# Kernel tuning notes

Measured on AMD Instinct MI355X. Metric: run time of the kernel, lower is better.

## Reference

```python
import jax, jax.numpy as jnp
import numpy as np

V = 50000      # vocabulary size (len(negative_sampling_table))
E = 256        # embedding_size
R = 180        # time_scope_radius -> 2R+1 = 361 time buckets
B = 2048       # batch
L = 200        # context length
NOPT = 10      # number of candidate targets (mixed_target has NOPT+1 cols)


def setup_inputs() -> dict:
    key = jax.random.key(0)
    k1, k2, k3, k4, k5, k6 = jax.random.split(key, 6)
    context = jax.random.randint(k1, (B, L, 2), 0, V, dtype=jnp.int64)
    mixed_target = jax.random.randint(k2, (B, NOPT + 1), 0, V, dtype=jnp.int64)
    context_emb_table = jax.random.normal(k3, (V, E), dtype=jnp.float32)
    target_emb_table = jax.random.normal(k4, (V, E), dtype=jnp.float32)
    taa_matrix = jax.random.uniform(k5, (V, 2 * R + 1), dtype=jnp.float32)
    taa_bias = jax.random.uniform(k6, (V, 1), dtype=jnp.float32)
    return {
        "context": context,
        "mixed_target": mixed_target,
        "context_emb_table": context_emb_table,
        "target_emb_table": target_emb_table,
        "taa_matrix": taa_matrix,
        "taa_bias": taa_bias,
    }


def reference(context, mixed_target, context_emb_table, target_emb_table, taa_matrix, taa_bias):
    radius = (taa_matrix.shape[1] - 1) // 2
    context_event = context[:, :, 0]          # [B, L]
    context_time = context[:, :, 1]           # [B, L]
    n_options = mixed_target.shape[-1] - 1
    target_event = mixed_target[:, :n_options]   # [B, n_options]
    target_time = mixed_target[:, n_options:]    # [B, 1]

    # mask padded positions (event id == -1)
    context_mask = jnp.where(context_event == -1, 0, 1)
    context_event = context_event * context_mask

    context_embedding = context_emb_table[context_event]          # [B, L, E]

    time_delta = jnp.clip(context_time - target_time + radius, 0, 2 * radius)  # [B, L]

    activated_taa = jax.nn.softmax(taa_matrix + taa_bias, axis=1)  # [V, 2R+1]
    taa_weights = activated_taa[context_event, time_delta]         # [B, L]

    # weighted masked sum over context positions
    w = taa_weights * context_mask.astype(taa_weights.dtype)       # [B, L]
    hidden = jnp.einsum("ble,bl->be", context_embedding, w)       # [B, E]

    target_embedding = target_emb_table[target_event]              # [B, n_options, E]
    scores = jnp.einsum("bne,be->bn", target_embedding, hidden)   # [B, n_options]
    return scores
```

## Files before the change

kernel.cpp:

```cpp
#include <hip/hip_runtime.h>
#include <hip/hip_bf16.h>

#define V 50000
#define E 256
#define RADIUS 180
#define TAA_W (2 * RADIUS + 1)
#define BATCH 2048
#define CTX_L 200
#define NOPT 10

#define ISE_GROUPS (V / 8)
#define VEC4_TOTAL (V * E / 4)
#define PREP_GRID  2048

typedef float vf4 __attribute__((ext_vector_type(4)));

__device__ __forceinline__ unsigned short f2bf_rne(float f) {
    unsigned u = __float_as_uint(f);
    u += 0x7fffu + ((u >> 16) & 1u);
    return (unsigned short)(u >> 16);
}
__device__ __forceinline__ unsigned pack_bf16(float a, float b) {
    return (unsigned)f2bf_rne(a) | ((unsigned)f2bf_rne(b) << 16);
}
__device__ __forceinline__ float bf_lo(unsigned u) {
    return __uint_as_float(u << 16);
}
__device__ __forceinline__ float bf_hi(unsigned u) {
    return __uint_as_float(u & 0xffff0000u);
}

__global__ __launch_bounds__(256) void prep_persist_kernel(
    const float* __restrict__ taa, const float* __restrict__ ctx_tab,
    float* __restrict__ inv, uint2* __restrict__ btab, int do_conv)
{
    __shared__ float s_e[8 * TAA_W];
    const int tid = threadIdx.x;

    for (int g = blockIdx.x; g < ISE_GROUPS; g += PREP_GRID) {
        const float4* p = (const float4*)taa + (size_t)g * 722;
#pragma unroll
        for (int k = 0; k < 3; ++k) {
            int j = tid + 256 * k;
            if (j < 722) {
                float4 v = p[j];
                float* d = &s_e[4 * j];
                d[0] = __expf(v.x);
                d[1] = __expf(v.y);
                d[2] = __expf(v.z);
                d[3] = __expf(v.w);
            }
        }
        __syncthreads();
        const int r = tid >> 5;
        const int c = tid & 31;
        const float* row = &s_e[r * TAA_W];
        float s = 0.f;
#pragma unroll
        for (int i = c; i < TAA_W; i += 32) s += row[i];
        for (int off = 1; off < 32; off <<= 1) s += __shfl_xor(s, off, 64);
        if (c == 0) inv[8 * g + r] = 1.0f / s;
        __syncthreads();
    }

    if (do_conv) {
        const vf4* src = (const vf4*)ctx_tab;
        size_t i = (size_t)blockIdx.x * 256 + tid;
        const size_t step = (size_t)PREP_GRID * 256;
        for (; i + step < VEC4_TOTAL; i += 2 * step) {
            vf4 va = __builtin_nontemporal_load(src + i);
            vf4 vb = __builtin_nontemporal_load(src + i + step);
            uint2 oa, ob;
            oa.x = pack_bf16(va.x, va.y);
            oa.y = pack_bf16(va.z, va.w);
            ob.x = pack_bf16(vb.x, vb.y);
            ob.y = pack_bf16(vb.z, vb.w);
            btab[i] = oa;
            btab[i + step] = ob;
        }
        if (i < VEC4_TOTAL) {
            vf4 v = __builtin_nontemporal_load(src + i);
            uint2 o;
            o.x = pack_bf16(v.x, v.y);
            o.y = pack_bf16(v.z, v.w);
            btab[i] = o;
        }
    }
}

template <int USE_BF16>
__global__ __launch_bounds__(256) void mce_taa_main_kernel(
    const int*   __restrict__ ctx,
    const int*   __restrict__ mt,
    const float* __restrict__ ctx_tab,
    const uint2* __restrict__ btab,
    const float* __restrict__ tgt_tab,
    const float* __restrict__ taa,
    const float* __restrict__ inv,
    float*       __restrict__ out)
{
    __shared__ int   s_ev[CTX_L];
    __shared__ float s_w[CTX_L];
    __shared__ float s_part[4 * E];
    __shared__ float s_hid[E];

    const int b   = blockIdx.x;
    const int tid = threadIdx.x;
    const int tgt_time = mt[b * (NOPT + 1) + NOPT];

    if (tid < CTX_L) {
        int2 ct = ((const int2*)ctx)[b * CTX_L + tid];
        int ev = ct.x, t = ct.y;
        int mask = (ev == -1) ? 0 : 1;
        ev = mask ? ev : 0;
        if (ev < 0) ev += V;
        int td = t - tgt_time + RADIUS;
        td = min(max(td, 0), 2 * RADIUS);
        float x = taa[(size_t)ev * TAA_W + td];
        s_ev[tid] = ev;
        s_w[tid]  = mask ? __expf(x) * inv[ev] : 0.f;
    }
    __syncthreads();

    const int ws   = tid >> 6;
    const int lane = tid & 63;

    float a0 = 0.f, a1 = 0.f, a2 = 0.f, a3 = 0.f;
    if (USE_BF16) {
#pragma unroll 3
        for (int l0 = 0; l0 < 192; l0 += 16) {
            int   la = l0 + ws,      lb = l0 + 4 + ws;
            int   lc = l0 + 8 + ws,  ld = l0 + 12 + ws;
            int   ea = s_ev[la], eb = s_ev[lb], ec = s_ev[lc], ed = s_ev[ld];
            float wa = s_w[la],  wb = s_w[lb],  wc = s_w[lc],  wd = s_w[ld];
            uint2 ua = btab[(size_t)ea * (E / 4) + lane];
            uint2 ub = btab[(size_t)eb * (E / 4) + lane];
            uint2 uc = btab[(size_t)ec * (E / 4) + lane];
            uint2 ud = btab[(size_t)ed * (E / 4) + lane];
            a0 = fmaf(bf_lo(ua.x), wa, a0);
            a1 = fmaf(bf_hi(ua.x), wa, a1);
            a2 = fmaf(bf_lo(ua.y), wa, a2);
            a3 = fmaf(bf_hi(ua.y), wa, a3);
            a0 = fmaf(bf_lo(ub.x), wb, a0);
            a1 = fmaf(bf_hi(ub.x), wb, a1);
            a2 = fmaf(bf_lo(ub.y), wb, a2);
            a3 = fmaf(bf_hi(ub.y), wb, a3);
            a0 = fmaf(bf_lo(uc.x), wc, a0);
            a1 = fmaf(bf_hi(uc.x), wc, a1);
            a2 = fmaf(bf_lo(uc.y), wc, a2);
            a3 = fmaf(bf_hi(uc.y), wc, a3);
            a0 = fmaf(bf_lo(ud.x), wd, a0);
            a1 = fmaf(bf_hi(ud.x), wd, a1);
            a2 = fmaf(bf_lo(ud.y), wd, a2);
            a3 = fmaf(bf_hi(ud.y), wd, a3);
        }
        {
            int   la = 192 + ws,     lb = 196 + ws;
            int   ea = s_ev[la],     eb = s_ev[lb];
            float wa = s_w[la],      wb = s_w[lb];
            uint2 ua = btab[(size_t)ea * (E / 4) + lane];
            uint2 ub = btab[(size_t)eb * (E / 4) + lane];
            a0 = fmaf(bf_lo(ua.x), wa, a0);
            a1 = fmaf(bf_hi(ua.x), wa, a1);
            a2 = fmaf(bf_lo(ua.y), wa, a2);
            a3 = fmaf(bf_hi(ua.y), wa, a3);
            a0 = fmaf(bf_lo(ub.x), wb, a0);
            a1 = fmaf(bf_hi(ub.x), wb, a1);
            a2 = fmaf(bf_lo(ub.y), wb, a2);
            a3 = fmaf(bf_hi(ub.y), wb, a3);
        }
    } else {
        const float4* tab4 = (const float4*)ctx_tab;
#pragma unroll 5
        for (int l0 = 0; l0 < CTX_L; l0 += 4) {
            int    l  = l0 + ws;
            int    ev = s_ev[l];
            float  w  = s_w[l];
            float4 u  = tab4[(size_t)ev * (E / 4) + lane];
            a0 = fmaf(u.x, w, a0);
            a1 = fmaf(u.y, w, a1);
            a2 = fmaf(u.z, w, a2);
            a3 = fmaf(u.w, w, a3);
        }
    }
    {
        float* p = &s_part[ws * E + lane * 4];
        p[0] = a0; p[1] = a1; p[2] = a2; p[3] = a3;
    }
    __syncthreads();
    s_hid[tid] = s_part[tid] + s_part[E + tid] + s_part[2 * E + tid] + s_part[3 * E + tid];
    __syncthreads();

    const float4* ttab4 = (const float4*)tgt_tab;
    for (int n = ws; n < NOPT; n += 4) {
        int tg = mt[b * (NOPT + 1) + n];
        if (tg < 0) tg += V;
        float4 u = ttab4[(size_t)tg * (E / 4) + lane];
        float p = u.x * s_hid[lane * 4 + 0]
                + u.y * s_hid[lane * 4 + 1]
                + u.z * s_hid[lane * 4 + 2]
                + u.w * s_hid[lane * 4 + 3];
        for (int off = 32; off > 0; off >>= 1) p += __shfl_xor(p, off, 64);
        if (lane == 0) out[b * NOPT + n] = p;
    }
}

extern "C" void kernel_launch(void* const* d_in, const int* in_sizes, int n_in,
                              void* d_out, int out_size, void* d_ws, size_t ws_size,
                              hipStream_t stream) {
    const int*   ctx     = (const int*)d_in[0];
    const int*   mt      = (const int*)d_in[1];
    const float* ctx_tab = (const float*)d_in[2];
    const float* tgt_tab = (const float*)d_in[3];
    const float* taa     = (const float*)d_in[4];
    float* out = (float*)d_out;

    float* inv  = (float*)d_ws;
    uint2* btab = (uint2*)((char*)d_ws + (256 << 10));
    const size_t need = (256 << 10) + (size_t)V * E * 2;
    const int use_bf16 = (ws_size >= need) ? 1 : 0;

    prep_persist_kernel<<<PREP_GRID, 256, 0, stream>>>(taa, ctx_tab, inv, btab,
                                                       use_bf16);
    if (use_bf16) {
        mce_taa_main_kernel<1><<<BATCH, 256, 0, stream>>>(
            ctx, mt, ctx_tab, btab, tgt_tab, taa, inv, out);
    } else {
        mce_taa_main_kernel<0><<<BATCH, 256, 0, stream>>>(
            ctx, mt, ctx_tab, btab, tgt_tab, taa, inv, out);
    }
}
```

Baseline: 215.2 us.

## Widen bf16 gathers to 16B, pack event/weight in LDS, prefetch targets

```diff
diff --git a/kernel.cpp b/kernel.cpp
--- a/kernel.cpp
+++ b/kernel.cpp
@@ -1,5 +1,4 @@
 #include <hip/hip_runtime.h>
-#include <hip/hip_bf16.h>
 
 #define V 50000
 #define E 256
@@ -14,6 +13,7 @@
 #define PREP_GRID  2048
 
 typedef float vf4 __attribute__((ext_vector_type(4)));
+typedef float v2f __attribute__((ext_vector_type(2)));
 
 __device__ __forceinline__ unsigned short f2bf_rne(float f) {
     unsigned u = __float_as_uint(f);
@@ -99,10 +99,10 @@
     const float* __restrict__ inv,
     float*       __restrict__ out)
 {
-    __shared__ int   s_ev[CTX_L];
-    __shared__ float s_w[CTX_L];
-    __shared__ float s_part[4 * E];
-    __shared__ float s_hid[E];
+    __shared__ float2 s_evw[CTX_L];
+    __shared__ float  s_part[4 * E];
+    __shared__ float  s_hid[E];
+    __shared__ float4 s_tgt[NOPT * (E / 4)];
 
     const int b   = blockIdx.x;
     const int tid = threadIdx.x;
@@ -117,73 +117,75 @@
         int td = t - tgt_time + RADIUS;
         td = min(max(td, 0), 2 * RADIUS);
         float x = taa[(size_t)ev * TAA_W + td];
-        s_ev[tid] = ev;
-        s_w[tid]  = mask ? __expf(x) * inv[ev] : 0.f;
+        float2 q;
+        q.x = __int_as_float(ev);
+        q.y = mask ? __expf(x) * inv[ev] : 0.f;
+        s_evw[tid] = q;
+    }
+    {
+        const float4* ttab4 = (const float4*)tgt_tab;
+#pragma unroll
+        for (int k = 0; k < 3; ++k) {
+            int idx = tid + 256 * k;
+            if (idx < NOPT * (E / 4)) {
+                int row = idx >> 6;
+                int col = idx & 63;
+                int tg  = mt[b * (NOPT + 1) + row];
+                if (tg < 0) tg += V;
+                s_tgt[idx] = ttab4[(size_t)tg * (E / 4) + col];
+            }
+        }
     }
     __syncthreads();
 
     const int ws   = tid >> 6;
     const int lane = tid & 63;
-
-    float a0 = 0.f, a1 = 0.f, a2 = 0.f, a3 = 0.f;
+    const int c    = lane & 31;
+    const int h    = lane >> 5;
+
     if (USE_BF16) {
-#pragma unroll 3
-        for (int l0 = 0; l0 < 192; l0 += 16) {
-            int   la = l0 + ws,      lb = l0 + 4 + ws;
-            int   lc = l0 + 8 + ws,  ld = l0 + 12 + ws;
-            int   ea = s_ev[la], eb = s_ev[lb], ec = s_ev[lc], ed = s_ev[ld];
-            float wa = s_w[la],  wb = s_w[lb],  wc = s_w[lc],  wd = s_w[ld];
-            uint2 ua = btab[(size_t)ea * (E / 4) + lane];
-            uint2 ub = btab[(size_t)eb * (E / 4) + lane];
-            uint2 uc = btab[(size_t)ec * (E / 4) + lane];
-            uint2 ud = btab[(size_t)ed * (E / 4) + lane];
-            a0 = fmaf(bf_lo(ua.x), wa, a0);
-            a1 = fmaf(bf_hi(ua.x), wa, a1);
-            a2 = fmaf(bf_lo(ua.y), wa, a2);
-            a3 = fmaf(bf_hi(ua.y), wa, a3);
-            a0 = fmaf(bf_lo(ub.x), wb, a0);
-            a1 = fmaf(bf_hi(ub.x), wb, a1);
-            a2 = fmaf(bf_lo(ub.y), wb, a2);
-            a3 = fmaf(bf_hi(ub.y), wb, a3);
-            a0 = fmaf(bf_lo(uc.x), wc, a0);
-            a1 = fmaf(bf_hi(uc.x), wc, a1);
-            a2 = fmaf(bf_lo(uc.y), wc, a2);
-            a3 = fmaf(bf_hi(uc.y), wc, a3);
-            a0 = fmaf(bf_lo(ud.x), wd, a0);
-            a1 = fmaf(bf_hi(ud.x), wd, a1);
-            a2 = fmaf(bf_lo(ud.y), wd, a2);
-            a3 = fmaf(bf_hi(ud.y), wd, a3);
-        }
-        {
-            int   la = 192 + ws,     lb = 196 + ws;
-            int   ea = s_ev[la],     eb = s_ev[lb];
-            float wa = s_w[la],      wb = s_w[lb];
-            uint2 ua = btab[(size_t)ea * (E / 4) + lane];
-            uint2 ub = btab[(size_t)eb * (E / 4) + lane];
-            a0 = fmaf(bf_lo(ua.x), wa, a0);
-            a1 = fmaf(bf_hi(ua.x), wa, a1);
-            a2 = fmaf(bf_lo(ua.y), wa, a2);
-            a3 = fmaf(bf_hi(ua.y), wa, a3);
-            a0 = fmaf(bf_lo(ub.x), wb, a0);
-            a1 = fmaf(bf_hi(ub.x), wb, a1);
-            a2 = fmaf(bf_lo(ub.y), wb, a2);
-            a3 = fmaf(bf_hi(ub.y), wb, a3);
+        v2f a01 = {0.f, 0.f}, a23 = {0.f, 0.f}, a45 = {0.f, 0.f}, a67 = {0.f, 0.f};
+        const uint4* bt4 = (const uint4*)btab;
+#pragma unroll 5
+        for (int it = 0; it < 25; ++it) {
+            int    l = 8 * it + 2 * ws + h;
+            float2 q = s_evw[l];
+            int    ev = __float_as_int(q.x);
+            float  w  = q.y;
+            uint4  u  = bt4[(size_t)ev * 32 + c];
+            v2f wv = {w, w};
+            v2f p0 = {bf_lo(u.x), bf_hi(u.x)};
+            v2f p1 = {bf_lo(u.y), bf_hi(u.y)};
+            v2f p2 = {bf_lo(u.z), bf_hi(u.z)};
+            v2f p3 = {bf_lo(u.w), bf_hi(u.w)};
+            a01 += p0 * wv;
+            a23 += p1 * wv;
+            a45 += p2 * wv;
+            a67 += p3 * wv;
+        }
+        float a[8] = {a01.x, a01.y, a23.x, a23.y, a45.x, a45.y, a67.x, a67.y};
+#pragma unroll
+        for (int k = 0; k < 8; ++k) a[k] += __shfl_xor(a[k], 32, 64);
+        if (h == 0) {
+            float* p = &s_part[ws * E + c * 8];
+#pragma unroll
+            for (int k = 0; k < 8; ++k) p[k] = a[k];
         }
     } else {
+        float a0 = 0.f, a1 = 0.f, a2 = 0.f, a3 = 0.f;
         const float4* tab4 = (const float4*)ctx_tab;
 #pragma unroll 5
         for (int l0 = 0; l0 < CTX_L; l0 += 4) {
             int    l  = l0 + ws;
-            int    ev = s_ev[l];
-            float  w  = s_w[l];
+            float2 q  = s_evw[l];
+            int    ev = __float_as_int(q.x);
+            float  w  = q.y;
             float4 u  = tab4[(size_t)ev * (E / 4) + lane];
             a0 = fmaf(u.x, w, a0);
             a1 = fmaf(u.y, w, a1);
             a2 = fmaf(u.z, w, a2);
             a3 = fmaf(u.w, w, a3);
         }
-    }
-    {
         float* p = &s_part[ws * E + lane * 4];
         p[0] = a0; p[1] = a1; p[2] = a2; p[3] = a3;
     }
@@ -191,11 +193,8 @@
     s_hid[tid] = s_part[tid] + s_part[E + tid] + s_part[2 * E + tid] + s_part[3 * E + tid];
     __syncthreads();
 
-    const float4* ttab4 = (const float4*)tgt_tab;
     for (int n = ws; n < NOPT; n += 4) {
-        int tg = mt[b * (NOPT + 1) + n];
-        if (tg < 0) tg += V;
-        float4 u = ttab4[(size_t)tg * (E / 4) + lane];
+        float4 u = s_tgt[n * (E / 4) + lane];
         float p = u.x * s_hid[lane * 4 + 0]
                 + u.y * s_hid[lane * 4 + 1]
                 + u.z * s_hid[lane * 4 + 2]
```

Result: no change. 215.8 us (+0.3%).
